# Performance work log

Hardware: AMD Instinct MI355X
Metric: run time of the kernel (lower is better)

The kernel has to match this reference:

```python
import jax, jax.numpy as jnp
import numpy as np

N_NODES = 50000
N_EDGES = 800000
N_GRAPHS = 512
IN_CH = 64
HID = 64
NEG_SLOPE = 0.2  # PyG GATConv default


def leaky_relu(x):
    return jnp.where(x >= 0, x, NEG_SLOPE * x)


def gat_conv(x, src, dst, W, a_src, a_dst, bias):
    # x: [N, in]; src/dst: [E] (self-loops already included)
    h = x @ W                                   # [N, hid]
    # per-edge attention logits (heads=1)
    alpha_s = h @ a_src                         # [N]
    alpha_d = h @ a_dst                         # [N]
    logits = leaky_relu(alpha_s[src] + alpha_d[dst])   # [E]
    # segment softmax over destination nodes
    seg_max = jax.ops.segment_max(logits, dst, num_segments=N_NODES)
    seg_max = jnp.where(jnp.isfinite(seg_max), seg_max, 0.0)
    ex = jnp.exp(logits - seg_max[dst])
    denom = jax.ops.segment_sum(ex, dst, num_segments=N_NODES)
    alpha = ex / jnp.maximum(denom[dst], 1e-16)
    # scatter-weighted aggregation of source features
    out = jax.ops.segment_sum(alpha[:, None] * h[src], dst, num_segments=N_NODES)
    return out + bias


def setup_inputs() -> dict:
    key = jax.random.key(0)
    ks = jax.random.split(key, 12)
    x = jax.random.normal(ks[0], (N_NODES, IN_CH), dtype=jnp.float32)
    edge_index = jax.random.randint(ks[1], (2, N_EDGES), 0, N_NODES, dtype=jnp.int64)
    batch = jnp.sort(jax.random.randint(ks[2], (N_NODES,), 0, N_GRAPHS, dtype=jnp.int64))
    s1 = 1.0 / np.sqrt(IN_CH)
    s2 = 1.0 / np.sqrt(HID)
    W1 = jax.random.normal(ks[3], (IN_CH, HID), dtype=jnp.float32) * s1
    a_src1 = jax.random.normal(ks[4], (HID,), dtype=jnp.float32) * s2
    a_dst1 = jax.random.normal(ks[5], (HID,), dtype=jnp.float32) * s2
    b1 = jnp.zeros((HID,), dtype=jnp.float32)
    W2 = jax.random.normal(ks[6], (HID, HID), dtype=jnp.float32) * s2
    a_src2 = jax.random.normal(ks[7], (HID,), dtype=jnp.float32) * s2
    a_dst2 = jax.random.normal(ks[8], (HID,), dtype=jnp.float32) * s2
    b2 = jnp.zeros((HID,), dtype=jnp.float32)
    return {"x": x, "edge_index": edge_index, "batch": batch,
            "W1": W1, "a_src1": a_src1, "a_dst1": a_dst1, "b1": b1,
            "W2": W2, "a_src2": a_src2, "a_dst2": a_dst2, "b2": b2}


def reference(x, edge_index, batch, W1, a_src1, a_dst1, b1, W2, a_src2, a_dst2, b2):
    # add self-loops (PyG GATConv default add_self_loops=True)
    loops = jnp.arange(N_NODES, dtype=edge_index.dtype)
    src = jnp.concatenate([edge_index[0], loops])
    dst = jnp.concatenate([edge_index[1], loops])
    h = jax.nn.elu(gat_conv(x, src, dst, W1, a_src1, a_dst1, b1))
    h = jax.nn.elu(gat_conv(h, src, dst, W2, a_src2, a_dst2, b2))
    # global mean pool per graph
    sums = jax.ops.segment_sum(h, batch, num_segments=N_GRAPHS)        # [G, hid]
    cnt = jax.ops.segment_sum(jnp.ones((N_NODES,), h.dtype), batch, num_segments=N_GRAPHS)
    return sums / jnp.maximum(cnt, 1.0)[:, None]
```

## Files before the change

kernel.cpp:

```cpp
#include <hip/hip_runtime.h>
#include <hip/hip_bf16.h>
#include <math.h>

#define N_NODES_C 50000
#define N_EDGES_C 800000
#define E_TOT_C   (N_EDGES_C + N_NODES_C)
#define N_GRAPHS_C 512
#define CH 64
#define NBUCK 391
#define NB_BUCK 256
#define BCAP 3328
#define TRF_NODES 32

__device__ __forceinline__ float wave_reduce_sum(float v) {
#pragma unroll
    for (int m = 32; m >= 1; m >>= 1) v += __shfl_xor(v, m, 64);
    return v;
}


__global__ __launch_bounds__(256) void prelim_kernel(
    const int* __restrict__ batch, int* __restrict__ gstart, int* __restrict__ bucket_cnt,
    const float* __restrict__ W1, const float* __restrict__ as1, const float* __restrict__ ad1,
    const float* __restrict__ W2, const float* __restrict__ as2, const float* __restrict__ ad2,
    float* __restrict__ wa)
{
    int blk = blockIdx.x, t = threadIdx.x;
    if (blk >= 196) {
        if (t < 64) {
            const float* W  = (blk == 196) ? W1  : W2;
            const float* As = (blk == 196) ? as1 : as2;
            const float* Ad = (blk == 196) ? ad1 : ad2;
            float ss = 0.f, dd = 0.f;
#pragma unroll 8
            for (int c = 0; c < 64; ++c) {
                float w = W[t * 64 + c];
                ss = fmaf(w, As[c], ss);
                dd = fmaf(w, Ad[c], dd);
            }
            float* o = wa + ((blk == 196) ? 0 : 128);
            o[t] = ss; o[64 + t] = dd;
        }
        return;
    }
    int i = blk * 256 + t;
    if (i < NBUCK) bucket_cnt[i] = 0;
    if (i >= N_NODES_C) return;
    int bcur = batch[i];
    int bprev = (i > 0) ? batch[i - 1] : -1;
    for (int g = bprev + 1; g <= bcur; ++g) gstart[g] = i;
    if (i == N_NODES_C - 1)
        for (int g = bcur + 1; g <= N_GRAPHS_C; ++g) gstart[g] = N_NODES_C;
}


__global__ __launch_bounds__(512) void bucket_build(const int* __restrict__ ei,
                                                    int* __restrict__ bucket_cnt,
                                                    unsigned int* __restrict__ buck_edges) {
    __shared__ int cnt[NBUCK];
    __shared__ int lbase[NBUCK];
    int t = threadIdx.x, blk = blockIdx.x;
    for (int i = t; i < NBUCK; i += 512) cnt[i] = 0;
    __syncthreads();
    const int CHUNK = (E_TOT_C + NB_BUCK - 1) / NB_BUCK;
    int beg = blk * CHUNK, end = min(beg + CHUNK, E_TOT_C);
    for (int e = beg + t; e < end; e += 512) {
        int d = (e < N_EDGES_C) ? ei[N_EDGES_C + e] : (e - N_EDGES_C);
        atomicAdd(&cnt[d >> 7], 1);
    }
    __syncthreads();
    for (int b = t; b < NBUCK; b += 512) {
        int c = cnt[b];
        lbase[b] = (c > 0) ? atomicAdd(&bucket_cnt[b], c) : 0;
        cnt[b] = 0;
    }
    __syncthreads();
    for (int e = beg + t; e < end; e += 512) {
        int s_, d_;
        if (e < N_EDGES_C) { s_ = ei[e]; d_ = ei[N_EDGES_C + e]; }
        else               { s_ = d_ = e - N_EDGES_C; }
        int b = d_ >> 7;
        int pos = lbase[b] + atomicAdd(&cnt[b], 1);
        buck_edges[b * BCAP + pos] = ((unsigned)(d_ & 127) << 16) | (unsigned)s_;
    }
}

__global__ __launch_bounds__(512) void bucket_to_csr(const unsigned int* __restrict__ buck_edges,
                                                     const int* __restrict__ bucket_cnt,
                                                     unsigned short* __restrict__ csr_src,
                                                     unsigned int* __restrict__ row_ptr) {
    __shared__ unsigned int ebuf[BCAP];
    __shared__ unsigned short sbuf[BCAP];
    __shared__ int deg[128], off[128], cur[128];
    __shared__ int wsum;
    int bb = blockIdx.x, t = threadIdx.x;
    int base = bb * BCAP;
    int size = min(bucket_cnt[bb], BCAP);
    int node0 = bb << 7;
    int nnodes = min(128, N_NODES_C - node0);
    for (int i = t; i < size; i += 512) ebuf[i] = buck_edges[base + i];
    if (t < 128) deg[t] = 0;
    __syncthreads();
    for (int i = t; i < size; i += 512) atomicAdd(&deg[(ebuf[i] >> 16) & 127], 1);
    __syncthreads();
    int myscan = 0;
    if (t < 128) {
        int l = t & 63;
        int s = deg[t];
#pragma unroll
        for (int o = 1; o < 64; o <<= 1) {
            int u = __shfl_up(s, o, 64);
            if (l >= o) s += u;
        }
        myscan = s;
        if (t == 63) wsum = s;
    }
    __syncthreads();
    if (t < 128) {
        int add = (t >= 64) ? wsum : 0;
        off[t] = myscan + add - deg[t];
        cur[t] = 0;
    }
    __syncthreads();
    for (int i = t; i < size; i += 512) {
        unsigned pk = ebuf[i];
        int l = (pk >> 16) & 127;
        int p = atomicAdd(&cur[l], 1);
        sbuf[off[l] + p] = (unsigned short)(pk & 0xFFFFu);
    }
    __syncthreads();
    for (int i = t; i < size; i += 512) csr_src[base + i] = sbuf[i];
    if (t < nnodes)
        row_ptr[node0 + t] = ((unsigned)(base + off[t]) << 8) | (unsigned)min(deg[t], 255);
}


__global__ __launch_bounds__(256) void transform_kernel(
    const float* __restrict__ xin, const float* __restrict__ W,
    const float* __restrict__ wa,
    __hip_bfloat16* __restrict__ hout, float* __restrict__ as_out,
    float* __restrict__ ad_out)
{
    __shared__ float Wl[64][64];
    __shared__ __align__(16) float xs[64][36];
    __shared__ float wsv[64], wdv[64];
    int t = threadIdx.x;
    const float4* W4 = (const float4*)W;
    float4* Wl4 = (float4*)&Wl[0][0];
    for (int i = t; i < 1024; i += 256) Wl4[i] = W4[i];
    if (t < 64) wsv[t] = wa[t];
    else if (t < 128) wdv[t - 64] = wa[t];
    int n0 = blockIdx.x * TRF_NODES;
    int nn = min(TRF_NODES, N_NODES_C - n0);
    if (nn < TRF_NODES) {
        for (int idx = t; idx < 64 * TRF_NODES; idx += 256) {
            int k = idx >> 5, row = idx & 31;
            if (row >= nn) xs[k][row] = 0.f;
        }
    }
    for (int idx = t; idx < nn * 16; idx += 256) {
        int row = idx >> 4, f4 = idx & 15;
        float4 v = *reinterpret_cast<const float4*>(xin + (size_t)(n0 + row) * CH + f4 * 4);
        xs[f4 * 4 + 0][row] = v.x;
        xs[f4 * 4 + 1][row] = v.y;
        xs[f4 * 4 + 2][row] = v.z;
        xs[f4 * 4 + 3][row] = v.w;
    }
    __syncthreads();
    int w = t >> 6, c = t & 63, lane = t & 63;
    int r0 = w * 8;
    float acc[8] = {0.f, 0.f, 0.f, 0.f, 0.f, 0.f, 0.f, 0.f};
#pragma unroll 16
    for (int k = 0; k < 64; ++k) {
        float wl = Wl[k][c];
        float4 xa = *reinterpret_cast<const float4*>(&xs[k][r0]);
        float4 xb = *reinterpret_cast<const float4*>(&xs[k][r0 + 4]);
        acc[0] = fmaf(xa.x, wl, acc[0]);
        acc[1] = fmaf(xa.y, wl, acc[1]);
        acc[2] = fmaf(xa.z, wl, acc[2]);
        acc[3] = fmaf(xa.w, wl, acc[3]);
        acc[4] = fmaf(xb.x, wl, acc[4]);
        acc[5] = fmaf(xb.y, wl, acc[5]);
        acc[6] = fmaf(xb.z, wl, acc[6]);
        acc[7] = fmaf(xb.w, wl, acc[7]);
    }
    size_t hb = (size_t)(n0 + r0) * CH + c;
#pragma unroll
    for (int i = 0; i < 8; ++i)
        if (r0 + i < nn) hout[hb + (size_t)i * CH] = __float2bfloat16(acc[i]);
    int kb = lane & 7;
    int rloc = r0 + (lane >> 3);
    float ps = 0.f, pd = 0.f;
#pragma unroll
    for (int j = 0; j < 8; ++j) {
        int k = kb + 8 * j;
        float xv = xs[k][rloc];
        ps = fmaf(xv, wsv[k], ps);
        pd = fmaf(xv, wdv[k], pd);
    }
#pragma unroll
    for (int m = 1; m <= 4; m <<= 1) {
        ps += __shfl_xor(ps, m, 64);
        pd += __shfl_xor(pd, m, 64);
    }
    if (kb == 0 && rloc < nn) {
        as_out[n0 + rloc] = ps;
        ad_out[n0 + rloc] = pd;
    }
}

__global__ __launch_bounds__(256) void aggregate_kernel(
    const __hip_bfloat16* __restrict__ h, const float* __restrict__ as,
    const float* __restrict__ ad, const float* __restrict__ bias,
    const unsigned int* __restrict__ row_ptr, const unsigned short* __restrict__ csr_src,
    float* __restrict__ out)
{
    int t = threadIdx.x;
    int w = t >> 6, lane = t & 63;
    int n = blockIdx.x * 4 + w;
    unsigned rp = row_ptr[n];
    int beg = (int)(rp >> 8);
    int deg = (int)(rp & 255u);
    float adn = ad[n];
    if (deg <= 64) {
        int s_reg = (int)csr_src[beg + min(lane, deg - 1)];
        float ex = 0.f;
        if (lane < deg) {
            float v = as[s_reg] + adn;
            v = (v >= 0.f) ? v : 0.2f * v;
            ex = __expf(v);
        }
        float ssum = wave_reduce_sum(ex);
        float inv = 1.f / fmaxf(ssum, 1e-16f);
        int sub = lane >> 3;
        int cg  = (lane & 7) << 3;
        float a0 = 0.f, a1 = 0.f, a2 = 0.f, a3 = 0.f;
        float a4 = 0.f, a5 = 0.f, a6 = 0.f, a7 = 0.f;
        int jmax = (deg + 15) >> 4;
        for (int j = 0; j < jmax; ++j) {
            int e1 = j * 16 + sub;
            int e2 = e1 + 8;
            int   s1 = __shfl(s_reg, e1, 64);
            int   s2 = __shfl(s_reg, e2, 64);
            float w1 = __shfl(ex, e1, 64);
            float w2 = __shfl(ex, e2, 64);
            uint4 u1 = make_uint4(0, 0, 0, 0), u2 = make_uint4(0, 0, 0, 0);
            if (e1 < deg) u1 = *reinterpret_cast<const uint4*>(h + (size_t)s1 * CH + cg);
            if (e2 < deg) u2 = *reinterpret_cast<const uint4*>(h + (size_t)s2 * CH + cg);
            a0 = fmaf(w1, __uint_as_float(u1.x << 16), a0);
            a1 = fmaf(w1, __uint_as_float(u1.x & 0xFFFF0000u), a1);
            a2 = fmaf(w1, __uint_as_float(u1.y << 16), a2);
            a3 = fmaf(w1, __uint_as_float(u1.y & 0xFFFF0000u), a3);
            a4 = fmaf(w1, __uint_as_float(u1.z << 16), a4);
            a5 = fmaf(w1, __uint_as_float(u1.z & 0xFFFF0000u), a5);
            a6 = fmaf(w1, __uint_as_float(u1.w << 16), a6);
            a7 = fmaf(w1, __uint_as_float(u1.w & 0xFFFF0000u), a7);
            a0 = fmaf(w2, __uint_as_float(u2.x << 16), a0);
            a1 = fmaf(w2, __uint_as_float(u2.x & 0xFFFF0000u), a1);
            a2 = fmaf(w2, __uint_as_float(u2.y << 16), a2);
            a3 = fmaf(w2, __uint_as_float(u2.y & 0xFFFF0000u), a3);
            a4 = fmaf(w2, __uint_as_float(u2.z << 16), a4);
            a5 = fmaf(w2, __uint_as_float(u2.z & 0xFFFF0000u), a5);
            a6 = fmaf(w2, __uint_as_float(u2.w << 16), a6);
            a7 = fmaf(w2, __uint_as_float(u2.w & 0xFFFF0000u), a7);
        }
#pragma unroll
        for (int msk = 8; msk <= 32; msk <<= 1) {
            a0 += __shfl_xor(a0, msk, 64); a1 += __shfl_xor(a1, msk, 64);
            a2 += __shfl_xor(a2, msk, 64); a3 += __shfl_xor(a3, msk, 64);
            a4 += __shfl_xor(a4, msk, 64); a5 += __shfl_xor(a5, msk, 64);
            a6 += __shfl_xor(a6, msk, 64); a7 += __shfl_xor(a7, msk, 64);
        }
        float v = a0;
        v = (sub == 1) ? a1 : v;
        v = (sub == 2) ? a2 : v;
        v = (sub == 3) ? a3 : v;
        v = (sub == 4) ? a4 : v;
        v = (sub == 5) ? a5 : v;
        v = (sub == 6) ? a6 : v;
        v = (sub == 7) ? a7 : v;
        int ch = cg | sub;
        v = v * inv + bias[ch];
        v = (v > 0.f) ? v : __expf(v) - 1.f;
        out[(size_t)n * CH + ch] = v;
    } else {
        int end = beg + deg;
        float ssum = 0.f;
        for (int i = beg + lane; i < end; i += 64) {
            float v = as[csr_src[i]] + adn;
            v = (v >= 0.f) ? v : 0.2f * v;
            ssum += __expf(v);
        }
        ssum = wave_reduce_sum(ssum);
        float inv = 1.f / fmaxf(ssum, 1e-16f);
        float acc = 0.f;
        for (int i = beg; i < end; ++i) {
            int s = csr_src[i];
            float v = as[s] + adn;
            v = (v >= 0.f) ? v : 0.2f * v;
            float ww = __expf(v);
            acc = fmaf(ww, __bfloat162float(h[(size_t)s * CH + lane]), acc);
        }
        acc = acc * inv + bias[lane];
        out[(size_t)n * CH + lane] = (acc > 0.f) ? acc : __expf(acc) - 1.f;
    }
}


__global__ __launch_bounds__(256) void pool_kernel(
    const float* __restrict__ h, const int* __restrict__ gstart,
    float* __restrict__ out)
{
    __shared__ float red[4][64];
    int g = blockIdx.x;
    int t = threadIdx.x, w = t >> 6, lane = t & 63;
    int beg = gstart[g], end = gstart[g + 1];
    float acc = 0.f;
    for (int n = beg + w; n < end; n += 4) acc += h[n * CH + lane];
    red[w][lane] = acc;
    __syncthreads();
    if (w == 0) {
        float v = red[0][lane] + red[1][lane] + red[2][lane] + red[3][lane];
        float c = (float)(end - beg);
        out[g * CH + lane] = v / fmaxf(c, 1.f);
    }
}


extern "C" void kernel_launch(void* const* d_in, const int* in_sizes, int n_in,
                              void* d_out, int out_size, void* d_ws, size_t ws_size,
                              hipStream_t stream)
{
    const float* x   = (const float*)d_in[0];
    const int*   ei  = (const int*)d_in[1];
    const int*   bat = (const int*)d_in[2];
    const float* W1  = (const float*)d_in[3];
    const float* as1 = (const float*)d_in[4];
    const float* ad1 = (const float*)d_in[5];
    const float* b1  = (const float*)d_in[6];
    const float* W2  = (const float*)d_in[7];
    const float* as2 = (const float*)d_in[8];
    const float* ad2 = (const float*)d_in[9];
    const float* b2  = (const float*)d_in[10];
    float* out = (float*)d_out;

    char* ws = (char*)d_ws;
    size_t off = 0;
    auto alloc = [&](size_t bytes) -> void* {
        void* p = ws + off;
        off += (bytes + 255) & ~size_t(255);
        return p;
    };
    __hip_bfloat16* hbuf = (__hip_bfloat16*)alloc(sizeof(__hip_bfloat16) * N_NODES_C * CH);
    float* obuf    = (float*)alloc(sizeof(float) * N_NODES_C * CH);
    float* alpha_s = (float*)alloc(sizeof(float) * N_NODES_C);
    float* alpha_d = (float*)alloc(sizeof(float) * N_NODES_C);
    int*   bucket_cnt = (int*)alloc(sizeof(int) * NBUCK);
    unsigned int* buck_edges = (unsigned int*)alloc(sizeof(unsigned) * NBUCK * BCAP);
    unsigned short* csr_src  = (unsigned short*)alloc(sizeof(unsigned short) * NBUCK * BCAP);
    unsigned int* row_ptr    = (unsigned int*)alloc(sizeof(unsigned) * N_NODES_C);
    int*   gstart  = (int*)alloc(sizeof(int) * (N_GRAPHS_C + 1));
    float* wa      = (float*)alloc(sizeof(float) * 256);

    const int NB_AGG = N_NODES_C / 4;
    const int NB_TRF = (N_NODES_C + TRF_NODES - 1) / TRF_NODES;

    prelim_kernel<<<198, 256, 0, stream>>>(bat, gstart, bucket_cnt,
                                           W1, as1, ad1, W2, as2, ad2, wa);
    bucket_build<<<NB_BUCK, 512, 0, stream>>>(ei, bucket_cnt, buck_edges);
    bucket_to_csr<<<NBUCK, 512, 0, stream>>>(buck_edges, bucket_cnt, csr_src, row_ptr);

    transform_kernel<<<NB_TRF, 256, 0, stream>>>(x, W1, wa, hbuf, alpha_s, alpha_d);
    aggregate_kernel<<<NB_AGG, 256, 0, stream>>>(hbuf, alpha_s, alpha_d, b1,
                                                 row_ptr, csr_src, obuf);
    transform_kernel<<<NB_TRF, 256, 0, stream>>>(obuf, W2, wa + 128, hbuf, alpha_s, alpha_d);
    aggregate_kernel<<<NB_AGG, 256, 0, stream>>>(hbuf, alpha_s, alpha_d, b2,
                                                 row_ptr, csr_src, obuf);

    pool_kernel<<<N_GRAPHS_C, 256, 0, stream>>>(obuf, gstart, out);
}
```

Before: 200.0 us.

## Fuse bucket build with first transform, enlarge transform tile, streamline aggregate reduction

Merges the edge bucketing kernel and the layer-1 feature transform into one launch, with blocks split by index and shared memory held in a union, so the independent work overlaps and one launch is saved. The transform tile grows from 32 to 64 nodes per block, giving each thread 16 accumulators. In aggregation, the full 16-edge groups drop their bounds checks and the remainder is handled separately. The 8-accumulator butterfly reduction is replaced by a transpose-style halving reduction that needs fewer shuffles. Risks are higher register and LDS use in the fused kernel and a build block count cut to 256 threads.

After: 180.2 us. 1.11x faster.

```diff
diff --git a/kernel.cpp b/kernel.cpp
--- a/kernel.cpp
+++ b/kernel.cpp
@@ -10,7 +10,8 @@
 #define NBUCK 391
 #define NB_BUCK 256
 #define BCAP 3328
-#define TRF_NODES 32
+#define TRF_NODES 64
+#define NB_TRF ((N_NODES_C + TRF_NODES - 1) / TRF_NODES)
 
 __device__ __forceinline__ float wave_reduce_sum(float v) {
 #pragma unroll
@@ -54,36 +55,143 @@
 }
 
 
-__global__ __launch_bounds__(512) void bucket_build(const int* __restrict__ ei,
-                                                    int* __restrict__ bucket_cnt,
-                                                    unsigned int* __restrict__ buck_edges) {
-    __shared__ int cnt[NBUCK];
-    __shared__ int lbase[NBUCK];
-    int t = threadIdx.x, blk = blockIdx.x;
-    for (int i = t; i < NBUCK; i += 512) cnt[i] = 0;
+struct TrfSmem {
+    float Wl[64][64];
+    __align__(16) float xs[64][68];
+    float wsv[64], wdv[64];
+};
+struct BuildSmem { int cnt[NBUCK]; int lbase[NBUCK]; };
+union __align__(16) FusedSmem { TrfSmem t; BuildSmem b; };
+
+
+__device__ __forceinline__ void build_body(
+    BuildSmem& sm, int blk, const int* __restrict__ ei,
+    int* __restrict__ bucket_cnt, unsigned int* __restrict__ buck_edges)
+{
+    int t = threadIdx.x;
+    for (int i = t; i < NBUCK; i += 256) sm.cnt[i] = 0;
     __syncthreads();
     const int CHUNK = (E_TOT_C + NB_BUCK - 1) / NB_BUCK;
     int beg = blk * CHUNK, end = min(beg + CHUNK, E_TOT_C);
-    for (int e = beg + t; e < end; e += 512) {
+    for (int e = beg + t; e < end; e += 256) {
         int d = (e < N_EDGES_C) ? ei[N_EDGES_C + e] : (e - N_EDGES_C);
-        atomicAdd(&cnt[d >> 7], 1);
-    }
-    __syncthreads();
-    for (int b = t; b < NBUCK; b += 512) {
-        int c = cnt[b];
-        lbase[b] = (c > 0) ? atomicAdd(&bucket_cnt[b], c) : 0;
-        cnt[b] = 0;
-    }
-    __syncthreads();
-    for (int e = beg + t; e < end; e += 512) {
+        atomicAdd(&sm.cnt[d >> 7], 1);
+    }
+    __syncthreads();
+    for (int b = t; b < NBUCK; b += 256) {
+        int c = sm.cnt[b];
+        sm.lbase[b] = (c > 0) ? atomicAdd(&bucket_cnt[b], c) : 0;
+        sm.cnt[b] = 0;
+    }
+    __syncthreads();
+    for (int e = beg + t; e < end; e += 256) {
         int s_, d_;
         if (e < N_EDGES_C) { s_ = ei[e]; d_ = ei[N_EDGES_C + e]; }
         else               { s_ = d_ = e - N_EDGES_C; }
         int b = d_ >> 7;
-        int pos = lbase[b] + atomicAdd(&cnt[b], 1);
+        int pos = sm.lbase[b] + atomicAdd(&sm.cnt[b], 1);
         buck_edges[b * BCAP + pos] = ((unsigned)(d_ & 127) << 16) | (unsigned)s_;
     }
 }
+
+
+__device__ __forceinline__ void transform_body(
+    TrfSmem& sm, int bb,
+    const float* __restrict__ xin, const float* __restrict__ W,
+    const float* __restrict__ wa,
+    __hip_bfloat16* __restrict__ hout, float* __restrict__ as_out,
+    float* __restrict__ ad_out)
+{
+    int t = threadIdx.x;
+    const float4* W4 = (const float4*)W;
+    float4* Wl4 = (float4*)&sm.Wl[0][0];
+    for (int i = t; i < 1024; i += 256) Wl4[i] = W4[i];
+    if (t < 64) sm.wsv[t] = wa[t];
+    else if (t < 128) sm.wdv[t - 64] = wa[t];
+    int n0 = bb * TRF_NODES;
+    int nn = min(TRF_NODES, N_NODES_C - n0);
+    if (nn < TRF_NODES) {
+        for (int idx = t; idx < 64 * TRF_NODES; idx += 256) {
+            int k = idx >> 6, row = idx & 63;
+            if (row >= nn) sm.xs[k][row] = 0.f;
+        }
+    }
+    for (int idx = t; idx < nn * 16; idx += 256) {
+        int row = idx >> 4, f4 = idx & 15;
+        float4 v = *reinterpret_cast<const float4*>(xin + (size_t)(n0 + row) * CH + f4 * 4);
+        sm.xs[f4 * 4 + 0][row] = v.x;
+        sm.xs[f4 * 4 + 1][row] = v.y;
+        sm.xs[f4 * 4 + 2][row] = v.z;
+        sm.xs[f4 * 4 + 3][row] = v.w;
+    }
+    __syncthreads();
+    int w = t >> 6, c = t & 63, lane = t & 63;
+    int r0 = w * 16;
+    float acc[16];
+#pragma unroll
+    for (int i = 0; i < 16; ++i) acc[i] = 0.f;
+#pragma unroll 8
+    for (int k = 0; k < 64; ++k) {
+        float wl = sm.Wl[k][c];
+        const float4* xp = reinterpret_cast<const float4*>(&sm.xs[k][r0]);
+        float4 xa = xp[0], xb = xp[1], xc = xp[2], xd = xp[3];
+        acc[0]  = fmaf(xa.x, wl, acc[0]);  acc[1]  = fmaf(xa.y, wl, acc[1]);
+        acc[2]  = fmaf(xa.z, wl, acc[2]);  acc[3]  = fmaf(xa.w, wl, acc[3]);
+        acc[4]  = fmaf(xb.x, wl, acc[4]);  acc[5]  = fmaf(xb.y, wl, acc[5]);
+        acc[6]  = fmaf(xb.z, wl, acc[6]);  acc[7]  = fmaf(xb.w, wl, acc[7]);
+        acc[8]  = fmaf(xc.x, wl, acc[8]);  acc[9]  = fmaf(xc.y, wl, acc[9]);
+        acc[10] = fmaf(xc.z, wl, acc[10]); acc[11] = fmaf(xc.w, wl, acc[11]);
+        acc[12] = fmaf(xd.x, wl, acc[12]); acc[13] = fmaf(xd.y, wl, acc[13]);
+        acc[14] = fmaf(xd.z, wl, acc[14]); acc[15] = fmaf(xd.w, wl, acc[15]);
+    }
+    size_t hb = (size_t)(n0 + r0) * CH + c;
+#pragma unroll
+    for (int i = 0; i < 16; ++i)
+        if (r0 + i < nn) hout[hb + (size_t)i * CH] = __float2bfloat16(acc[i]);
+    int kb = lane & 3;
+    int rloc = r0 + (lane >> 2);
+    float ps = 0.f, pd = 0.f;
+#pragma unroll
+    for (int j = 0; j < 16; ++j) {
+        int k = kb + 4 * j;
+        float xv = sm.xs[k][rloc];
+        ps = fmaf(xv, sm.wsv[k], ps);
+        pd = fmaf(xv, sm.wdv[k], pd);
+    }
+    ps += __shfl_xor(ps, 1, 64); ps += __shfl_xor(ps, 2, 64);
+    pd += __shfl_xor(pd, 1, 64); pd += __shfl_xor(pd, 2, 64);
+    if (kb == 0 && rloc < nn) {
+        as_out[n0 + rloc] = ps;
+        ad_out[n0 + rloc] = pd;
+    }
+}
+
+
+__global__ __launch_bounds__(256) void fused_build_trf(
+    const int* __restrict__ ei, int* __restrict__ bucket_cnt,
+    unsigned int* __restrict__ buck_edges,
+    const float* __restrict__ xin, const float* __restrict__ W,
+    const float* __restrict__ wa,
+    __hip_bfloat16* __restrict__ hout, float* __restrict__ as_out,
+    float* __restrict__ ad_out)
+{
+    __shared__ FusedSmem sm;
+    if (blockIdx.x < NB_BUCK)
+        build_body(sm.b, blockIdx.x, ei, bucket_cnt, buck_edges);
+    else
+        transform_body(sm.t, blockIdx.x - NB_BUCK, xin, W, wa, hout, as_out, ad_out);
+}
+
+__global__ __launch_bounds__(256) void transform_kernel(
+    const float* __restrict__ xin, const float* __restrict__ W,
+    const float* __restrict__ wa,
+    __hip_bfloat16* __restrict__ hout, float* __restrict__ as_out,
+    float* __restrict__ ad_out)
+{
+    __shared__ TrfSmem sm;
+    transform_body(sm, blockIdx.x, xin, W, wa, hout, as_out, ad_out);
+}
+
 
 __global__ __launch_bounds__(512) void bucket_to_csr(const unsigned int* __restrict__ buck_edges,
                                                      const int* __restrict__ bucket_cnt,
@@ -135,80 +243,6 @@
 }
 
 
-__global__ __launch_bounds__(256) void transform_kernel(
-    const float* __restrict__ xin, const float* __restrict__ W,
-    const float* __restrict__ wa,
-    __hip_bfloat16* __restrict__ hout, float* __restrict__ as_out,
-    float* __restrict__ ad_out)
-{
-    __shared__ float Wl[64][64];
-    __shared__ __align__(16) float xs[64][36];
-    __shared__ float wsv[64], wdv[64];
-    int t = threadIdx.x;
-    const float4* W4 = (const float4*)W;
-    float4* Wl4 = (float4*)&Wl[0][0];
-    for (int i = t; i < 1024; i += 256) Wl4[i] = W4[i];
-    if (t < 64) wsv[t] = wa[t];
-    else if (t < 128) wdv[t - 64] = wa[t];
-    int n0 = blockIdx.x * TRF_NODES;
-    int nn = min(TRF_NODES, N_NODES_C - n0);
-    if (nn < TRF_NODES) {
-        for (int idx = t; idx < 64 * TRF_NODES; idx += 256) {
-            int k = idx >> 5, row = idx & 31;
-            if (row >= nn) xs[k][row] = 0.f;
-        }
-    }
-    for (int idx = t; idx < nn * 16; idx += 256) {
-        int row = idx >> 4, f4 = idx & 15;
-        float4 v = *reinterpret_cast<const float4*>(xin + (size_t)(n0 + row) * CH + f4 * 4);
-        xs[f4 * 4 + 0][row] = v.x;
-        xs[f4 * 4 + 1][row] = v.y;
-        xs[f4 * 4 + 2][row] = v.z;
-        xs[f4 * 4 + 3][row] = v.w;
-    }
-    __syncthreads();
-    int w = t >> 6, c = t & 63, lane = t & 63;
-    int r0 = w * 8;
-    float acc[8] = {0.f, 0.f, 0.f, 0.f, 0.f, 0.f, 0.f, 0.f};
-#pragma unroll 16
-    for (int k = 0; k < 64; ++k) {
-        float wl = Wl[k][c];
-        float4 xa = *reinterpret_cast<const float4*>(&xs[k][r0]);
-        float4 xb = *reinterpret_cast<const float4*>(&xs[k][r0 + 4]);
-        acc[0] = fmaf(xa.x, wl, acc[0]);
-        acc[1] = fmaf(xa.y, wl, acc[1]);
-        acc[2] = fmaf(xa.z, wl, acc[2]);
-        acc[3] = fmaf(xa.w, wl, acc[3]);
-        acc[4] = fmaf(xb.x, wl, acc[4]);
-        acc[5] = fmaf(xb.y, wl, acc[5]);
-        acc[6] = fmaf(xb.z, wl, acc[6]);
-        acc[7] = fmaf(xb.w, wl, acc[7]);
-    }
-    size_t hb = (size_t)(n0 + r0) * CH + c;
-#pragma unroll
-    for (int i = 0; i < 8; ++i)
-        if (r0 + i < nn) hout[hb + (size_t)i * CH] = __float2bfloat16(acc[i]);
-    int kb = lane & 7;
-    int rloc = r0 + (lane >> 3);
-    float ps = 0.f, pd = 0.f;
-#pragma unroll
-    for (int j = 0; j < 8; ++j) {
-        int k = kb + 8 * j;
-        float xv = xs[k][rloc];
-        ps = fmaf(xv, wsv[k], ps);
-        pd = fmaf(xv, wdv[k], pd);
-    }
-#pragma unroll
-    for (int m = 1; m <= 4; m <<= 1) {
-        ps += __shfl_xor(ps, m, 64);
-        pd += __shfl_xor(pd, m, 64);
-    }
-    if (kb == 0 && rloc < nn) {
-        as_out[n0 + rloc] = ps;
-        ad_out[n0 + rloc] = pd;
-    }
-}
-
 __global__ __launch_bounds__(256) void aggregate_kernel(
     const __hip_bfloat16* __restrict__ h, const float* __restrict__ as,
     const float* __restrict__ ad, const float* __restrict__ bias,
@@ -223,6 +257,10 @@
     int deg = (int)(rp & 255u);
     float adn = ad[n];
     if (deg <= 64) {
+        int sub = lane >> 3;
+        int cg  = (lane & 7) << 3;
+        int ch  = cg | sub;
+        float bch = bias[ch];
         int s_reg = (int)csr_src[beg + min(lane, deg - 1)];
         float ex = 0.f;
         if (lane < deg) {
@@ -232,21 +270,18 @@
         }
         float ssum = wave_reduce_sum(ex);
         float inv = 1.f / fmaxf(ssum, 1e-16f);
-        int sub = lane >> 3;
-        int cg  = (lane & 7) << 3;
         float a0 = 0.f, a1 = 0.f, a2 = 0.f, a3 = 0.f;
         float a4 = 0.f, a5 = 0.f, a6 = 0.f, a7 = 0.f;
-        int jmax = (deg + 15) >> 4;
-        for (int j = 0; j < jmax; ++j) {
+        int full = deg >> 4, rem = deg & 15;
+        for (int j = 0; j < full; ++j) {
             int e1 = j * 16 + sub;
             int e2 = e1 + 8;
             int   s1 = __shfl(s_reg, e1, 64);
             int   s2 = __shfl(s_reg, e2, 64);
             float w1 = __shfl(ex, e1, 64);
             float w2 = __shfl(ex, e2, 64);
-            uint4 u1 = make_uint4(0, 0, 0, 0), u2 = make_uint4(0, 0, 0, 0);
-            if (e1 < deg) u1 = *reinterpret_cast<const uint4*>(h + (size_t)s1 * CH + cg);
-            if (e2 < deg) u2 = *reinterpret_cast<const uint4*>(h + (size_t)s2 * CH + cg);
+            uint4 u1 = *reinterpret_cast<const uint4*>(h + (size_t)s1 * CH + cg);
+            uint4 u2 = *reinterpret_cast<const uint4*>(h + (size_t)s2 * CH + cg);
             a0 = fmaf(w1, __uint_as_float(u1.x << 16), a0);
             a1 = fmaf(w1, __uint_as_float(u1.x & 0xFFFF0000u), a1);
             a2 = fmaf(w1, __uint_as_float(u1.y << 16), a2);
@@ -264,23 +299,54 @@
             a6 = fmaf(w2, __uint_as_float(u2.w << 16), a6);
             a7 = fmaf(w2, __uint_as_float(u2.w & 0xFFFF0000u), a7);
         }
-#pragma unroll
-        for (int msk = 8; msk <= 32; msk <<= 1) {
-            a0 += __shfl_xor(a0, msk, 64); a1 += __shfl_xor(a1, msk, 64);
-            a2 += __shfl_xor(a2, msk, 64); a3 += __shfl_xor(a3, msk, 64);
-            a4 += __shfl_xor(a4, msk, 64); a5 += __shfl_xor(a5, msk, 64);
-            a6 += __shfl_xor(a6, msk, 64); a7 += __shfl_xor(a7, msk, 64);
-        }
-        float v = a0;
-        v = (sub == 1) ? a1 : v;
-        v = (sub == 2) ? a2 : v;
-        v = (sub == 3) ? a3 : v;
-        v = (sub == 4) ? a4 : v;
-        v = (sub == 5) ? a5 : v;
-        v = (sub == 6) ? a6 : v;
-        v = (sub == 7) ? a7 : v;
-        int ch = cg | sub;
-        v = v * inv + bias[ch];
+        if (rem) {
+            int e1 = full * 16 + sub;
+            int   s1 = __shfl(s_reg, e1, 64);
+            float w1 = __shfl(ex, e1, 64);
+            uint4 u1 = make_uint4(0, 0, 0, 0);
+            if (e1 < deg) u1 = *reinterpret_cast<const uint4*>(h + (size_t)s1 * CH + cg);
+            a0 = fmaf(w1, __uint_as_float(u1.x << 16), a0);
+            a1 = fmaf(w1, __uint_as_float(u1.x & 0xFFFF0000u), a1);
+            a2 = fmaf(w1, __uint_as_float(u1.y << 16), a2);
+            a3 = fmaf(w1, __uint_as_float(u1.y & 0xFFFF0000u), a3);
+            a4 = fmaf(w1, __uint_as_float(u1.z << 16), a4);
+            a5 = fmaf(w1, __uint_as_float(u1.z & 0xFFFF0000u), a5);
+            a6 = fmaf(w1, __uint_as_float(u1.w << 16), a6);
+            a7 = fmaf(w1, __uint_as_float(u1.w & 0xFFFF0000u), a7);
+            if (rem > 8) {
+                int e2 = e1 + 8;
+                int   s2 = __shfl(s_reg, e2, 64);
+                float w2 = __shfl(ex, e2, 64);
+                uint4 u2 = make_uint4(0, 0, 0, 0);
+                if (e2 < deg) u2 = *reinterpret_cast<const uint4*>(h + (size_t)s2 * CH + cg);
+                a0 = fmaf(w2, __uint_as_float(u2.x << 16), a0);
+                a1 = fmaf(w2, __uint_as_float(u2.x & 0xFFFF0000u), a1);
+                a2 = fmaf(w2, __uint_as_float(u2.y << 16), a2);
+                a3 = fmaf(w2, __uint_as_float(u2.y & 0xFFFF0000u), a3);
+                a4 = fmaf(w2, __uint_as_float(u2.z << 16), a4);
+                a5 = fmaf(w2, __uint_as_float(u2.z & 0xFFFF0000u), a5);
+                a6 = fmaf(w2, __uint_as_float(u2.w << 16), a6);
+                a7 = fmaf(w2, __uint_as_float(u2.w & 0xFFFF0000u), a7);
+            }
+        }
+        bool hi5 = (lane & 32) != 0;
+        float t0 = __shfl_xor(hi5 ? a0 : a4, 32, 64);
+        float t1 = __shfl_xor(hi5 ? a1 : a5, 32, 64);
+        float t2 = __shfl_xor(hi5 ? a2 : a6, 32, 64);
+        float t3 = __shfl_xor(hi5 ? a3 : a7, 32, 64);
+        float b0 = (hi5 ? a4 : a0) + t0;
+        float b1 = (hi5 ? a5 : a1) + t1;
+        float b2 = (hi5 ? a6 : a2) + t2;
+        float b3 = (hi5 ? a7 : a3) + t3;
+        bool hi4 = (lane & 16) != 0;
+        float u0 = __shfl_xor(hi4 ? b0 : b2, 16, 64);
+        float u1s = __shfl_xor(hi4 ? b1 : b3, 16, 64);
+        float c0 = (hi4 ? b2 : b0) + u0;
+        float c1 = (hi4 ? b3 : b1) + u1s;
+        bool hi3 = (lane & 8) != 0;
+        float v1 = __shfl_xor(hi3 ? c0 : c1, 8, 64);
+        float r  = (hi3 ? c1 : c0) + v1;
+        float v = r * inv + bch;
         v = (v > 0.f) ? v : __expf(v) - 1.f;
         out[(size_t)n * CH + ch] = v;
     } else {
@@ -363,14 +429,13 @@
     float* wa      = (float*)alloc(sizeof(float) * 256);
 
     const int NB_AGG = N_NODES_C / 4;
-    const int NB_TRF = (N_NODES_C + TRF_NODES - 1) / TRF_NODES;
 
     prelim_kernel<<<198, 256, 0, stream>>>(bat, gstart, bucket_cnt,
                                            W1, as1, ad1, W2, as2, ad2, wa);
-    bucket_build<<<NB_BUCK, 512, 0, stream>>>(ei, bucket_cnt, buck_edges);
+    fused_build_trf<<<NB_BUCK + NB_TRF, 256, 0, stream>>>(ei, bucket_cnt, buck_edges,
+                                                          x, W1, wa, hbuf, alpha_s, alpha_d);
     bucket_to_csr<<<NBUCK, 512, 0, stream>>>(buck_edges, bucket_cnt, csr_src, row_ptr);
 
-    transform_kernel<<<NB_TRF, 256, 0, stream>>>(x, W1, wa, hbuf, alpha_s, alpha_d);
     aggregate_kernel<<<NB_AGG, 256, 0, stream>>>(hbuf, alpha_s, alpha_d, b1,
                                                  row_ptr, csr_src, obuf);
     transform_kernel<<<NB_TRF, 256, 0, stream>>>(obuf, W2, wa + 128, hbuf, alpha_s, alpha_d);
```
